# Optimization experiments

Measured on AMD Instinct MI355X. Metric: run time of the kernel, lower is better.

The kernel has to match this reference:

```python
import jax, jax.numpy as jnp
import numpy as np

N_NODES = 100_000
E_OFF = 1_000_000
HID = 32
GF = 8
NF = 8
N_LAYERS = 3


def _mlp(h, W1, b1, W2, b2):
    # Linear -> ReLU -> Linear (matches MLP([in, hidden, out]))
    return jax.nn.relu(h @ W1 + b1) @ W2 + b2


def _seg_mean(v, idx, n):
    s = jax.ops.segment_sum(v, idx, num_segments=n)
    c = jax.ops.segment_sum(jnp.ones((v.shape[0], 1), v.dtype), idx, num_segments=n)
    return s / jnp.maximum(c, 1.0)


def _graphnet(x, row, col, eattr2, g, p):
    # GraphNet with global block: edge MLP -> mean-aggregate to nodes -> node MLP -> global MLP
    eW1, eb1, eW2, eb2, nW1, nb1, nW2, nb2, gW1, gb1, gW2, gb2 = p
    n, e = x.shape[0], row.shape[0]
    gE = jnp.broadcast_to(g, (e, g.shape[1]))
    e_emb = _mlp(jnp.concatenate([gE, x[row], x[col], eattr2], axis=1), eW1, eb1, eW2, eb2)
    agg = _seg_mean(e_emb, row, n)
    gN = jnp.broadcast_to(g, (n, g.shape[1]))
    n_emb = _mlp(jnp.concatenate([gN, x, agg], axis=1), nW1, nb1, nW2, nb2)
    g_new = _mlp(jnp.concatenate([n_emb.mean(0, keepdims=True), e_emb.mean(0, keepdims=True), g], axis=1),
                 gW1, gb1, gW2, gb2)
    return e_emb, n_emb, g_new


def setup_inputs() -> dict:
    key = jax.random.key(0)
    ks = jax.random.split(key, 24)
    a = jax.random.randint(ks[0], (E_OFF,), 0, N_NODES)
    b = jax.random.randint(ks[1], (E_OFF,), 0, N_NODES)
    d = jnp.arange(N_NODES)
    l_ei = jnp.stack([jnp.concatenate([jnp.maximum(a, b), d]),
                      jnp.concatenate([jnp.minimum(a, b), d])])  # lower triangular + diag
    c = jax.random.randint(ks[2], (E_OFF,), 0, N_NODES)
    e = jax.random.randint(ks[3], (E_OFF,), 0, N_NODES)
    u_ei = jnp.stack([jnp.concatenate([jnp.minimum(c, e), d]),
                      jnp.concatenate([jnp.maximum(c, e), d])])  # upper triangular + diag
    E = E_OFF + N_NODES
    x = jax.random.normal(ks[4], (N_NODES, NF), dtype=jnp.float32)
    l_attr = jax.random.normal(ks[5], (E, 1), dtype=jnp.float32)
    u_attr = jax.random.normal(ks[6], (E, 1), dtype=jnp.float32)

    def w(k, shape):
        return (jax.random.normal(k, shape, dtype=jnp.float32) / np.sqrt(shape[-2])).astype(jnp.float32)

    e_in = GF + 2 * NF + 1 + 1  # 26 (edge attr padded to 2: skip col, zeros where absent)
    n_in = GF + 1 + NF          # 17
    g_in = NF + 1 + GF          # 17
    return {
        'x': x, 'l_edge_index': l_ei, 'u_edge_index': u_ei,
        'l_edge_attr': l_attr, 'u_edge_attr': u_attr,
        'eW1': w(ks[7], (2, N_LAYERS, e_in, HID)), 'eb1': 0.01 * jax.random.normal(ks[8], (2, N_LAYERS, HID)),
        'eW2': w(ks[9], (2, N_LAYERS, HID, 1)), 'eb2': 0.01 * jax.random.normal(ks[10], (2, N_LAYERS, 1)),
        'nW1': w(ks[11], (2, N_LAYERS, n_in, HID)), 'nb1': 0.01 * jax.random.normal(ks[12], (2, N_LAYERS, HID)),
        'nW2': w(ks[13], (2, N_LAYERS, HID, NF)), 'nb2': 0.01 * jax.random.normal(ks[14], (2, N_LAYERS, NF)),
        'gW1': w(ks[15], (2, N_LAYERS, g_in, HID)), 'gb1': 0.01 * jax.random.normal(ks[16], (2, N_LAYERS, HID)),
        'gW2': w(ks[17], (2, N_LAYERS, HID, GF)), 'gb2': 0.01 * jax.random.normal(ks[18], (2, N_LAYERS, GF)),
    }


def reference(x, l_edge_index, u_edge_index, l_edge_attr, u_edge_attr,
              eW1, eb1, eW2, eb2, nW1, nb1, nW2, nb2, gW1, gb1, gW2, gb2):
    params = (eW1, eb1, eW2, eb2, nW1, nb1, nW2, nb2, gW1, gb1, gW2, gb2)
    lr, lc = l_edge_index[0], l_edge_index[1]
    ur, uc = u_edge_index[0], u_edge_index[1]
    g = jnp.zeros((1, GF), x.dtype)
    l_e, u_e = l_edge_attr, u_edge_attr
    l_a = l_edge_attr  # skip-connection edge features (original matrix values)
    zl, zu = jnp.zeros_like(l_edge_attr), jnp.zeros_like(u_edge_attr)
    for i in range(N_LAYERS):
        p1 = tuple(w[0, i] for w in params)
        p2 = tuple(w[1, i] for w in params)
        l_in = jnp.concatenate([l_e, l_a if i != 0 else zl], axis=1)  # zeros col == no skip (block 0)
        l_e, l_n, g = _graphnet(x, lr, lc, l_in, g, p1)
        u_in = jnp.concatenate([u_e, zu], axis=1)  # l2 never has skip; padded zeros col
        u_e, u_n, g = _graphnet(l_n, ur, uc, u_in, g, p2)
        # NOTE: node embeddings are NOT carried across MP blocks in the original
    l_vals = jnp.where(lr == lc, jnp.exp(l_e[:, 0]), l_e[:, 0])
    u_vals = jnp.where(ur == uc, jnp.exp(u_e[:, 0]), u_e[:, 0])
    return jnp.concatenate([l_vals, u_vals])
```

## Files before the change

kernel.cpp:

```cpp
#include <hip/hip_runtime.h>


typedef unsigned int u32;

#define NB_SHIFT 9
#define NB_SIZE 512
#define RSTRIDE 1104

__device__ __forceinline__ float wave_sum(float v) {
#pragma unroll
    for (int off = 32; off > 0; off >>= 1) v += __shfl_down(v, off, 64);
    return v;
}


__global__ __launch_bounds__(256) void hist_kernel(
    const int* __restrict__ lr, const int* __restrict__ ur,
    u32* __restrict__ hist, int E, int B) {
    __shared__ u32 h[256];
    const int t = threadIdx.x;
    if (t < B) h[t] = 0;
    __syncthreads();
    const int s = blockIdx.y;
    const int* rows = s ? ur : lr;
    for (int i = blockIdx.x * 256 + t; i < E; i += gridDim.x * 256)
        atomicAdd(&h[rows[i] >> NB_SHIFT], 1u);
    __syncthreads();
    if (t < B && h[t]) atomicAdd(&hist[s * B + t], h[t]);
}

__global__ __launch_bounds__(256) void scan_kernel(
    const u32* __restrict__ hist, u32* __restrict__ offs,
    u32* __restrict__ cur, int B) {
    __shared__ u32 sh[256];
    const int t = threadIdx.x;
    for (int s = 0; s < 2; ++s) {
        const u32 v = (t < B) ? hist[s * B + t] : 0u;
        sh[t] = v;
        __syncthreads();
#pragma unroll
        for (int off = 1; off < 256; off <<= 1) {
            const u32 add = (t >= off) ? sh[t - off] : 0u;
            __syncthreads();
            sh[t] += add;
            __syncthreads();
        }
        const u32 exc = sh[t] - v;
        if (t < B) {
            offs[s * (B + 1) + t] = exc;
            cur[s * B + t] = exc;
        }
        if (t == 255) offs[s * (B + 1) + B] = sh[255];
        __syncthreads();
    }
}

#define SCHUNK 4096
__global__ __launch_bounds__(256) void scatter_kernel(
    const int* __restrict__ lr, const int* __restrict__ lc,
    const int* __restrict__ ur, const int* __restrict__ uc,
    const float* __restrict__ la, const float* __restrict__ ua,
    u32* __restrict__ cur, uint4* __restrict__ einfo, int E, int B) {
    __shared__ u32 lcnt[256], lbase[256];
    const int t = threadIdx.x;
    const int s = blockIdx.y;
    const int* rows = s ? ur : lr;
    const int* cols = s ? uc : lc;
    const float* attr = s ? ua : la;
    uint4* my = einfo + (size_t)s * E;
    if (t < B) lcnt[t] = 0;
    __syncthreads();
    const int base_e = blockIdx.x * SCHUNK;
#pragma unroll
    for (int k = 0; k < SCHUNK / 256; ++k) {
        const int e = base_e + k * 256 + t;
        if (e < E) atomicAdd(&lcnt[rows[e] >> NB_SHIFT], 1u);
    }
    __syncthreads();
    if (t < B) {
        const u32 c = lcnt[t];
        lbase[t] = c ? atomicAdd(&cur[s * B + t], c) : 0u;
        lcnt[t] = 0;
    }
    __syncthreads();
#pragma unroll
    for (int k = 0; k < SCHUNK / 256; ++k) {
        const int e = base_e + k * 256 + t;
        if (e < E) {
            const int r = rows[e];
            const int b = r >> NB_SHIFT;
            const u32 pos = lbase[b] + atomicAdd(&lcnt[b], 1u);
            my[pos] = make_uint4((u32)r, (u32)cols[e], (u32)e,
                                 __float_as_uint(attr[e]));
        }
    }
}


template <bool SKIP, bool FIRST, bool GAGG, bool VALS, bool STORE, bool GCOMP>
__global__ __launch_bounds__(512) void edge_kernel(
    const uint4* __restrict__ einfo,
    const float4* __restrict__ xf,
    const u32* __restrict__ offs,
    const float* __restrict__ eprev,
    const float* __restrict__ W1,
    const float* __restrict__ b1,
    const float* __restrict__ W2,
    const float* __restrict__ b2,
    const float* __restrict__ gprev,
    float* __restrict__ gout,
    const float* __restrict__ pebins,
    const float* __restrict__ pnbins,
    const float* __restrict__ gW1, const float* __restrict__ gb1,
    const float* __restrict__ gW2, const float* __restrict__ gb2,
    float* __restrict__ ebins,
    float* __restrict__ e_out,
    float* __restrict__ vals_out,
    int N, float inv_E) {
    __shared__ float asw[NB_SIZE * 32];
    const int t = threadIdx.x;
    const int b = blockIdx.x >> 1;

    if constexpr (GCOMP) {
        if (t < 64) {
            float nb[8];
#pragma unroll
            for (int q = 0; q < 8; ++q) nb[q] = pnbins[t * 16 + q];
            const float eb = pebins[t];
            float gin[17];
#pragma unroll
            for (int q = 0; q < 8; ++q) {
                const float s = wave_sum(nb[q]);
                gin[q] = __shfl(s, 0, 64) / (float)N;
            }
            const float es = wave_sum(eb);
            gin[8] = __shfl(es, 0, 64) * inv_E;
#pragma unroll
            for (int k = 0; k < 8; ++k) gin[9 + k] = gprev[k];
            float hv = 0.0f;
            if (t < 32) {
                hv = gb1[t];
#pragma unroll
                for (int k = 0; k < 17; ++k)
                    hv = fmaf(gin[k], gW1[k * 32 + t], hv);
                hv = fmaxf(hv, 0.0f);
            }
#pragma unroll
            for (int q = 0; q < 8; ++q) {
                const float c = (t < 32) ? hv * gW2[t * 8 + q] : 0.0f;
                const float s = wave_sum(c);
                if (t == 0) {
                    const float gv = gb2[q] + s;
                    asw[q] = gv;
                    if (blockIdx.x == 0) gout[q] = gv;
                }
            }
        }
    } else {
        if (t < 8) asw[t] = gprev[t];
    }
    __syncthreads();
    float gr[8];
#pragma unroll
    for (int k = 0; k < 8; ++k) gr[k] = asw[k];
    __syncthreads();

    const int n = (b << NB_SHIFT) + t;
    if (n < N) {
        const float4 x0 = xf[2 * (size_t)n], x1 = xf[2 * (size_t)n + 1];
        const float xs[8] = {x0.x, x0.y, x0.z, x0.w, x1.x, x1.y, x1.z, x1.w};
        float a[32];
#pragma unroll
        for (int j = 0; j < 32; ++j) {
            float v = b1[j];
#pragma unroll
            for (int k = 0; k < 8; ++k) v = fmaf(gr[k], W1[k * 32 + j], v);
            a[j] = v;
        }
        const float* __restrict__ WA = W1 + 8 * 32;
#pragma unroll
        for (int k = 0; k < 8; ++k) {
            const float v = xs[k];
#pragma unroll
            for (int j = 0; j < 32; ++j) a[j] = fmaf(v, WA[k * 32 + j], a[j]);
        }
        const int base = t * 32;
        const int sw = (t & 7) << 2;
#pragma unroll
        for (int q = 0; q < 8; ++q) {
            *(float4*)&asw[base + ((q * 4) ^ sw)] =
                make_float4(a[4 * q], a[4 * q + 1], a[4 * q + 2], a[4 * q + 3]);
        }
    }
    __syncthreads();

    const u32 beg = offs[b], end = offs[b + 1];
    const u32 len = end - beg;
    const u32 h0 = (len + 1) >> 1;
    const u32 hb = beg + ((blockIdx.x & 1) ? h0 : 0);
    const u32 he = (blockIdx.x & 1) ? end : beg + h0;
    const float* __restrict__ Wc = W1 + 16 * 32;
    const float* __restrict__ W24 = W1 + 24 * 32;
    const float* __restrict__ W25 = W1 + 25 * 32;
    float lsum = 0.0f;
    for (u32 i = hb + t; i < he; i += 512) {
        const uint4 e4 = einfo[i];
        const float attr = __uint_as_float(e4.w);
        float epv;
        if constexpr (FIRST) epv = attr;
        else epv = eprev[i];
        const u32 rl = e4.x & (NB_SIZE - 1);
        const int abase = rl * 32;
        const int asw_ = (rl & 7) << 2;
        float4 av[8];
#pragma unroll
        for (int q = 0; q < 8; ++q)
            av[q] = *(const float4*)&asw[abase + ((q * 4) ^ asw_)];
        const float4 xc0 = xf[2 * (size_t)e4.y];
        const float4 xc1 = xf[2 * (size_t)e4.y + 1];
        const float cx[8] = {xc0.x, xc0.y, xc0.z, xc0.w,
                             xc1.x, xc1.y, xc1.z, xc1.w};
        float hr[32];
#pragma unroll
        for (int q = 0; q < 8; ++q) {
            hr[4 * q + 0] = av[q].x; hr[4 * q + 1] = av[q].y;
            hr[4 * q + 2] = av[q].z; hr[4 * q + 3] = av[q].w;
        }
#pragma unroll
        for (int k = 0; k < 8; ++k) {
            const float v = cx[k];
#pragma unroll
            for (int j = 0; j < 32; ++j) hr[j] = fmaf(v, Wc[k * 32 + j], hr[j]);
        }
#pragma unroll
        for (int j = 0; j < 32; ++j) hr[j] = fmaf(epv, W24[j], hr[j]);
        if constexpr (SKIP) {
#pragma unroll
            for (int j = 0; j < 32; ++j) hr[j] = fmaf(attr, W25[j], hr[j]);
        }
        float out = b2[0];
#pragma unroll
        for (int j = 0; j < 32; ++j)
            out = fmaf(fmaxf(hr[j], 0.0f), W2[j], out);
        if constexpr (STORE) e_out[i] = out;
        if constexpr (VALS)
            vals_out[e4.z] = (e4.x == e4.y) ? expf(out) : out;
        if constexpr (GAGG) lsum += out;
    }
    if constexpr (GAGG) {
        __syncthreads();
        const float s = wave_sum(lsum);
        if ((t & 63) == 0) asw[t >> 6] = s;
        __syncthreads();
        if (t == 0) {
            float tot = 0.0f;
#pragma unroll
            for (int w = 0; w < 8; ++w) tot += asw[w];
            atomicAdd(&ebins[blockIdx.x & 63], tot);
        }
    }
}


template <bool COUNT, bool STORE_N>
__global__ __launch_bounds__(1024) void aggnode_kernel(
    const float* __restrict__ ep,
    const uint4* __restrict__ einfo,
    const u32* __restrict__ offs,
    const float4* __restrict__ xf,
    float* __restrict__ cntf,
    const float* __restrict__ g,
    const float* __restrict__ nW1, const float* __restrict__ nb1,
    const float* __restrict__ nW2, const float* __restrict__ nb2,
    float* __restrict__ n_out,
    float* __restrict__ nbins,
    int N) {
    __shared__ float sbin[NB_SIZE];
    __shared__ float cbin[NB_SIZE];
    __shared__ float biasN[32];
    __shared__ float npart[8][8];
    const int t = threadIdx.x;
    if (t < NB_SIZE) {
        sbin[t] = 0.0f;
        if constexpr (COUNT) cbin[t] = 0.0f;
    }
    if (t >= NB_SIZE && t < NB_SIZE + 32) {
        const int j = t - NB_SIZE;
        float v = nb1[j];
#pragma unroll
        for (int k = 0; k < 8; ++k) v = fmaf(g[k], nW1[k * 32 + j], v);
        biasN[j] = v;
    }
    __syncthreads();
    const int b = blockIdx.x;
    const u32 beg = offs[b], end = offs[b + 1];
    for (u32 i = beg + t; i < end; i += 1024) {
        const float v = ep[i];
        const u32 rl = einfo[i].x & (NB_SIZE - 1);
        atomicAdd(&sbin[rl], v);
        if constexpr (COUNT) atomicAdd(&cbin[rl], 1.0f);
    }
    __syncthreads();

    const int n0 = b << NB_SHIFT;
    float o[8];
    const bool active = (t < NB_SIZE) && (n0 + t < N);
    if (t < NB_SIZE) {
        const int n = n0 + t;
        const int idx = active ? n : (N - 1);
        float cntv;
        if constexpr (COUNT) {
            cntv = cbin[t];
            if (active) cntf[n] = cntv;
        } else {
            cntv = cntf[idx];
        }
        const float agg = sbin[t] / fmaxf(cntv, 1.0f);
        const float4 x0 = xf[2 * idx], x1 = xf[2 * idx + 1];
        float in[9] = {x0.x, x0.y, x0.z, x0.w, x1.x, x1.y, x1.z, x1.w, agg};
        float h[32];
#pragma unroll
        for (int j = 0; j < 8; ++j) {
            const float4 bb = reinterpret_cast<const float4*>(biasN)[j];
            h[4 * j + 0] = bb.x; h[4 * j + 1] = bb.y;
            h[4 * j + 2] = bb.z; h[4 * j + 3] = bb.w;
        }
        const float* __restrict__ Wk = nW1 + 8 * 32;
#pragma unroll
        for (int k = 0; k < 9; ++k) {
            const float v = in[k];
#pragma unroll
            for (int j = 0; j < 32; ++j) h[j] = fmaf(v, Wk[k * 32 + j], h[j]);
        }
#pragma unroll
        for (int q = 0; q < 8; ++q) o[q] = nb2[q];
#pragma unroll
        for (int j = 0; j < 32; ++j) {
            const float hv = fmaxf(h[j], 0.0f);
#pragma unroll
            for (int q = 0; q < 8; ++q) o[q] = fmaf(hv, nW2[j * 8 + q], o[q]);
        }
        if constexpr (STORE_N) {
            if (active) {
                reinterpret_cast<float4*>(n_out)[2 * n] =
                    make_float4(o[0], o[1], o[2], o[3]);
                reinterpret_cast<float4*>(n_out)[2 * n + 1] =
                    make_float4(o[4], o[5], o[6], o[7]);
            }
        }
#pragma unroll
        for (int q = 0; q < 8; ++q) {
            const float s = wave_sum(active ? o[q] : 0.0f);
            if ((t & 63) == 0) npart[t >> 6][q] = s;
        }
    }
    __syncthreads();
    if (t < 8) {
        float a = 0.0f;
#pragma unroll
        for (int w = 0; w < 8; ++w) a += npart[w][t];
        atomicAdd(&nbins[(b & 63) * 16 + t], a);
    }
}

extern "C" void kernel_launch(void* const* d_in, const int* in_sizes, int n_in,
                              void* d_out, int out_size, void* d_ws,
                              size_t ws_size, hipStream_t stream) {
    const float* x = (const float*)d_in[0];
    const int* l_ei = (const int*)d_in[1];
    const int* u_ei = (const int*)d_in[2];
    const float* l_attr = (const float*)d_in[3];
    const float* u_attr = (const float*)d_in[4];
    const float* eW1 = (const float*)d_in[5];
    const float* eb1 = (const float*)d_in[6];
    const float* eW2 = (const float*)d_in[7];
    const float* eb2 = (const float*)d_in[8];
    const float* nW1 = (const float*)d_in[9];
    const float* nb1 = (const float*)d_in[10];
    const float* nW2 = (const float*)d_in[11];
    const float* nb2 = (const float*)d_in[12];
    const float* gW1 = (const float*)d_in[13];
    const float* gb1 = (const float*)d_in[14];
    const float* gW2 = (const float*)d_in[15];
    const float* gb2 = (const float*)d_in[16];

    const int E = in_sizes[3];
    const int N = in_sizes[0] / 8;
    const int B = (N + NB_SIZE - 1) >> NB_SHIFT;
    const int Ep = (E + 3) & ~3;

    uint4* einfo = (uint4*)d_ws;
    float* l_e = (float*)(einfo + (size_t)2 * E);
    float* u_e = l_e + Ep;
    float* l_n = u_e + Ep;
    float* cnt_l = l_n + (size_t)8 * N;
    float* cnt_u = cnt_l + N;
    float* gslot = cnt_u + N;
    u32* hist = (u32*)(gslot + 56);
    float* dyn_all = (float*)(hist + 2 * B);
    u32* offs = (u32*)(dyn_all + 5 * RSTRIDE);
    u32* cur = offs + 2 * (B + 1);

    const int* lr = l_ei;
    const int* lc = l_ei + E;
    const int* ur = u_ei;
    const int* uc = u_ei + E;
    const int sg = (E + SCHUNK - 1) / SCHUNK;
    const float invE = 1.0f / (float)E;
    float* outL = (float*)d_out;
    float* outU = outL + E;
    const u32* offs_l = offs;
    const u32* offs_u = offs + (B + 1);

    hipMemsetAsync(gslot, 0, (size_t)(56 + 2 * B + 5 * RSTRIDE) * sizeof(float),
                   stream);
    hist_kernel<<<dim3(128, 2), 256, 0, stream>>>(lr, ur, hist, E, B);
    scan_kernel<<<1, 256, 0, stream>>>(hist, offs, cur, B);
    scatter_kernel<<<dim3(sg, 2), 256, 0, stream>>>(lr, lc, ur, uc, l_attr,
                                                    u_attr, cur, einfo, E, B);

    const size_t wsl[6] = {0, 3, 1, 4, 2, 5};

    for (int j = 0; j < 6; ++j) {
        const bool lower = !(j & 1);
        const size_t sl = wsl[j];
        float* ebins = dyn_all + (size_t)(j <= 4 ? j : 4) * RSTRIDE;
        float* nbins = ebins + 64;
        const float* pe = (j >= 1) ? dyn_all + (size_t)(j - 1) * RSTRIDE : nullptr;
        const float* pn = (j >= 1) ? pe + 64 : nullptr;
        const size_t psl = (j >= 1) ? wsl[j - 1] : 0;
        const float4* exf = (const float4*)(lower ? x : l_n);
        const uint4* einfo_t = einfo + (size_t)(lower ? 0 : 1) * E;
        const u32* eoffs = lower ? offs_l : offs_u;
        const float* eprev = lower ? l_e : u_e;
        float* e_out = lower ? l_e : u_e;
        const float* gprev = gslot + (size_t)(j >= 1 ? j - 1 : 0) * 8;
        float* gout = gslot + (size_t)j * 8;

#define EDGE_ARGS                                                             \
    einfo_t, exf, eoffs, eprev, eW1 + sl * 832, eb1 + sl * 32,                \
        eW2 + sl * 32, eb2 + sl, gprev, gout, pe, pn, gW1 + psl * 544,        \
        gb1 + psl * 32, gW2 + psl * 256, gb2 + psl * 8, ebins, e_out,         \
        (j == 4) ? outL : outU, N, invE

        switch (j) {
            case 0: edge_kernel<false, true, true, false, true, false>
                        <<<2 * B, 512, 0, stream>>>(EDGE_ARGS); break;
            case 1: edge_kernel<false, true, true, false, true, true>
                        <<<2 * B, 512, 0, stream>>>(EDGE_ARGS); break;
            case 2: edge_kernel<true, false, true, false, true, true>
                        <<<2 * B, 512, 0, stream>>>(EDGE_ARGS); break;
            case 3: edge_kernel<false, false, true, false, true, true>
                        <<<2 * B, 512, 0, stream>>>(EDGE_ARGS); break;
            case 4: edge_kernel<true, false, true, true, true, true>
                        <<<2 * B, 512, 0, stream>>>(EDGE_ARGS); break;
            case 5: edge_kernel<false, false, false, true, false, true>
                        <<<2 * B, 512, 0, stream>>>(EDGE_ARGS); break;
        }
#undef EDGE_ARGS

        if (j == 5) break;

        float* cntf = lower ? cnt_l : cnt_u;
        const float4* nxf = (const float4*)(lower ? x : l_n);

#define AGG_ARGS                                                              \
    e_out, einfo_t, eoffs, nxf, cntf, gslot + (size_t)j * 8, nW1 + sl * 544,  \
        nb1 + sl * 32, nW2 + sl * 256, nb2 + sl * 8, l_n, nbins, N

        switch (j) {
            case 0: aggnode_kernel<true, true>
                        <<<B, 1024, 0, stream>>>(AGG_ARGS); break;
            case 1: aggnode_kernel<true, false>
                        <<<B, 1024, 0, stream>>>(AGG_ARGS); break;
            case 2: aggnode_kernel<false, true>
                        <<<B, 1024, 0, stream>>>(AGG_ARGS); break;
            case 3: aggnode_kernel<false, false>
                        <<<B, 1024, 0, stream>>>(AGG_ARGS); break;
            case 4: aggnode_kernel<false, true>
                        <<<B, 1024, 0, stream>>>(AGG_ARGS); break;
        }
#undef AGG_ARGS
    }
}
```

Baseline: 606.4 us.

## Precompute per-node edge-MLP partials into a global table; flatten edge kernel grid

Splits the edge kernel. A new node kernel computes each node's row-side first-layer partial (global plus x[row] terms) once and writes it to a global table. The edge kernel then becomes a flat per-edge grid of 256-thread blocks that gathers that table instead of rebuilding it in LDS per bucket. Node buckets shrink from 512 to 256 with matching block sizes in the hist, scan, scatter and aggregation kernels. This trades LDS recomputation and uneven per-bucket load for an extra launch and a 32-float-per-node global gather per edge.

```diff
diff --git a/kernel.cpp b/kernel.cpp
--- a/kernel.cpp
+++ b/kernel.cpp
@@ -3,8 +3,8 @@
 
 typedef unsigned int u32;
 
-#define NB_SHIFT 9
-#define NB_SIZE 512
+#define NB_SHIFT 8
+#define NB_SIZE 256
 #define RSTRIDE 1104
 
 __device__ __forceinline__ float wave_sum(float v) {
@@ -14,32 +14,32 @@
 }
 
 
-__global__ __launch_bounds__(256) void hist_kernel(
+__global__ __launch_bounds__(512) void hist_kernel(
     const int* __restrict__ lr, const int* __restrict__ ur,
     u32* __restrict__ hist, int E, int B) {
-    __shared__ u32 h[256];
+    __shared__ u32 h[512];
     const int t = threadIdx.x;
     if (t < B) h[t] = 0;
     __syncthreads();
     const int s = blockIdx.y;
     const int* rows = s ? ur : lr;
-    for (int i = blockIdx.x * 256 + t; i < E; i += gridDim.x * 256)
+    for (int i = blockIdx.x * 512 + t; i < E; i += gridDim.x * 512)
         atomicAdd(&h[rows[i] >> NB_SHIFT], 1u);
     __syncthreads();
     if (t < B && h[t]) atomicAdd(&hist[s * B + t], h[t]);
 }
 
-__global__ __launch_bounds__(256) void scan_kernel(
+__global__ __launch_bounds__(512) void scan_kernel(
     const u32* __restrict__ hist, u32* __restrict__ offs,
     u32* __restrict__ cur, int B) {
-    __shared__ u32 sh[256];
+    __shared__ u32 sh[512];
     const int t = threadIdx.x;
     for (int s = 0; s < 2; ++s) {
         const u32 v = (t < B) ? hist[s * B + t] : 0u;
         sh[t] = v;
         __syncthreads();
 #pragma unroll
-        for (int off = 1; off < 256; off <<= 1) {
+        for (int off = 1; off < 512; off <<= 1) {
             const u32 add = (t >= off) ? sh[t - off] : 0u;
             __syncthreads();
             sh[t] += add;
@@ -50,18 +50,18 @@
             offs[s * (B + 1) + t] = exc;
             cur[s * B + t] = exc;
         }
-        if (t == 255) offs[s * (B + 1) + B] = sh[255];
+        if (t == 511) offs[s * (B + 1) + B] = sh[511];
         __syncthreads();
     }
 }
 
 #define SCHUNK 4096
-__global__ __launch_bounds__(256) void scatter_kernel(
+__global__ __launch_bounds__(512) void scatter_kernel(
     const int* __restrict__ lr, const int* __restrict__ lc,
     const int* __restrict__ ur, const int* __restrict__ uc,
     const float* __restrict__ la, const float* __restrict__ ua,
     u32* __restrict__ cur, uint4* __restrict__ einfo, int E, int B) {
-    __shared__ u32 lcnt[256], lbase[256];
+    __shared__ u32 lcnt[512], lbase[512];
     const int t = threadIdx.x;
     const int s = blockIdx.y;
     const int* rows = s ? ur : lr;
@@ -72,8 +72,8 @@
     __syncthreads();
     const int base_e = blockIdx.x * SCHUNK;
 #pragma unroll
-    for (int k = 0; k < SCHUNK / 256; ++k) {
-        const int e = base_e + k * 256 + t;
+    for (int k = 0; k < SCHUNK / 512; ++k) {
+        const int e = base_e + k * 512 + t;
         if (e < E) atomicAdd(&lcnt[rows[e] >> NB_SHIFT], 1u);
     }
     __syncthreads();
@@ -84,8 +84,8 @@
     }
     __syncthreads();
 #pragma unroll
-    for (int k = 0; k < SCHUNK / 256; ++k) {
-        const int e = base_e + k * 256 + t;
+    for (int k = 0; k < SCHUNK / 512; ++k) {
+        const int e = base_e + k * 512 + t;
         if (e < E) {
             const int r = rows[e];
             const int b = r >> NB_SHIFT;
@@ -97,30 +97,19 @@
 }
 
 
-template <bool SKIP, bool FIRST, bool GAGG, bool VALS, bool STORE, bool GCOMP>
-__global__ __launch_bounds__(512) void edge_kernel(
-    const uint4* __restrict__ einfo,
-    const float4* __restrict__ xf,
-    const u32* __restrict__ offs,
-    const float* __restrict__ eprev,
-    const float* __restrict__ W1,
+template <bool GCOMP>
+__global__ __launch_bounds__(256) void nodew_kernel(
+    const float4* __restrict__ xf, const float* __restrict__ W1,
     const float* __restrict__ b1,
-    const float* __restrict__ W2,
-    const float* __restrict__ b2,
     const float* __restrict__ gprev,
     float* __restrict__ gout,
     const float* __restrict__ pebins,
     const float* __restrict__ pnbins,
     const float* __restrict__ gW1, const float* __restrict__ gb1,
     const float* __restrict__ gW2, const float* __restrict__ gb2,
-    float* __restrict__ ebins,
-    float* __restrict__ e_out,
-    float* __restrict__ vals_out,
-    int N, float inv_E) {
-    __shared__ float asw[NB_SIZE * 32];
-    const int t = threadIdx.x;
-    const int b = blockIdx.x >> 1;
-
+    float4* __restrict__ Atab, int N, float inv_E) {
+    __shared__ float gsh[8];
+    const int t = threadIdx.x;
     if constexpr (GCOMP) {
         if (t < 64) {
             float nb[8];
@@ -151,119 +140,119 @@
                 const float s = wave_sum(c);
                 if (t == 0) {
                     const float gv = gb2[q] + s;
-                    asw[q] = gv;
+                    gsh[q] = gv;
                     if (blockIdx.x == 0) gout[q] = gv;
                 }
             }
         }
     } else {
-        if (t < 8) asw[t] = gprev[t];
-    }
-    __syncthreads();
+        if (t < 8) gsh[t] = gprev[t];
+    }
+    __syncthreads();
+    const int n = blockIdx.x * 256 + t;
+    if (n >= N) return;
     float gr[8];
 #pragma unroll
-    for (int k = 0; k < 8; ++k) gr[k] = asw[k];
-    __syncthreads();
-
-    const int n = (b << NB_SHIFT) + t;
-    if (n < N) {
-        const float4 x0 = xf[2 * (size_t)n], x1 = xf[2 * (size_t)n + 1];
-        const float xs[8] = {x0.x, x0.y, x0.z, x0.w, x1.x, x1.y, x1.z, x1.w};
-        float a[32];
-#pragma unroll
-        for (int j = 0; j < 32; ++j) {
-            float v = b1[j];
-#pragma unroll
-            for (int k = 0; k < 8; ++k) v = fmaf(gr[k], W1[k * 32 + j], v);
-            a[j] = v;
-        }
-        const float* __restrict__ WA = W1 + 8 * 32;
-#pragma unroll
-        for (int k = 0; k < 8; ++k) {
-            const float v = xs[k];
-#pragma unroll
-            for (int j = 0; j < 32; ++j) a[j] = fmaf(v, WA[k * 32 + j], a[j]);
-        }
-        const int base = t * 32;
-        const int sw = (t & 7) << 2;
-#pragma unroll
-        for (int q = 0; q < 8; ++q) {
-            *(float4*)&asw[base + ((q * 4) ^ sw)] =
-                make_float4(a[4 * q], a[4 * q + 1], a[4 * q + 2], a[4 * q + 3]);
-        }
-    }
-    __syncthreads();
-
-    const u32 beg = offs[b], end = offs[b + 1];
-    const u32 len = end - beg;
-    const u32 h0 = (len + 1) >> 1;
-    const u32 hb = beg + ((blockIdx.x & 1) ? h0 : 0);
-    const u32 he = (blockIdx.x & 1) ? end : beg + h0;
+    for (int k = 0; k < 8; ++k) gr[k] = gsh[k];
+    const float4 x0 = xf[2 * (size_t)n], x1 = xf[2 * (size_t)n + 1];
+    const float xs[8] = {x0.x, x0.y, x0.z, x0.w, x1.x, x1.y, x1.z, x1.w};
+    float a[32];
+#pragma unroll
+    for (int j = 0; j < 32; ++j) {
+        float v = b1[j];
+#pragma unroll
+        for (int k = 0; k < 8; ++k) v = fmaf(gr[k], W1[k * 32 + j], v);
+        a[j] = v;
+    }
+    const float* __restrict__ WA = W1 + 8 * 32;
+#pragma unroll
+    for (int k = 0; k < 8; ++k) {
+        const float v = xs[k];
+#pragma unroll
+        for (int j = 0; j < 32; ++j) a[j] = fmaf(v, WA[k * 32 + j], a[j]);
+    }
+    float4* An = Atab + 8 * (size_t)n;
+#pragma unroll
+    for (int q = 0; q < 8; ++q)
+        An[q] = make_float4(a[4 * q], a[4 * q + 1], a[4 * q + 2], a[4 * q + 3]);
+}
+
+
+template <bool SKIP, bool FIRST, bool GAGG, bool VALS, bool STORE>
+__global__ __launch_bounds__(256) void edge_kernel(
+    const uint4* __restrict__ einfo,
+    const float4* __restrict__ Atab,
+    const float4* __restrict__ xf,
+    const float* __restrict__ eprev,
+    const float* __restrict__ W1,
+    const float* __restrict__ W2,
+    const float* __restrict__ b2,
+    float* __restrict__ ebins,
+    float* __restrict__ e_out,
+    float* __restrict__ vals_out,
+    int E, int cpx) {
+    __shared__ float wpart[4];
+    const int t = threadIdx.x;
+    const int lid = (blockIdx.x & 7) * cpx + (blockIdx.x >> 3);
+    const int i0 = lid * 256;
+    if (i0 >= E) return;
+    const int i = i0 + t;
+    const bool valid = i < E;
+    const int idx = valid ? i : i0;
+
+    const uint4 e4 = einfo[idx];
+    const float attr = __uint_as_float(e4.w);
+    float epv;
+    if constexpr (FIRST) epv = attr;
+    else epv = eprev[idx];
+    const float4* __restrict__ Ar = Atab + 8 * (size_t)e4.x;
+    float h[32];
+#pragma unroll
+    for (int q = 0; q < 8; ++q) {
+        const float4 av = Ar[q];
+        h[4 * q + 0] = av.x; h[4 * q + 1] = av.y;
+        h[4 * q + 2] = av.z; h[4 * q + 3] = av.w;
+    }
+    const float4 xc0 = xf[2 * (size_t)e4.y], xc1 = xf[2 * (size_t)e4.y + 1];
+    const float cx[8] = {xc0.x, xc0.y, xc0.z, xc0.w,
+                         xc1.x, xc1.y, xc1.z, xc1.w};
     const float* __restrict__ Wc = W1 + 16 * 32;
+#pragma unroll
+    for (int k = 0; k < 8; ++k) {
+        const float v = cx[k];
+#pragma unroll
+        for (int j = 0; j < 32; ++j) h[j] = fmaf(v, Wc[k * 32 + j], h[j]);
+    }
     const float* __restrict__ W24 = W1 + 24 * 32;
-    const float* __restrict__ W25 = W1 + 25 * 32;
-    float lsum = 0.0f;
-    for (u32 i = hb + t; i < he; i += 512) {
-        const uint4 e4 = einfo[i];
-        const float attr = __uint_as_float(e4.w);
-        float epv;
-        if constexpr (FIRST) epv = attr;
-        else epv = eprev[i];
-        const u32 rl = e4.x & (NB_SIZE - 1);
-        const int abase = rl * 32;
-        const int asw_ = (rl & 7) << 2;
-        float4 av[8];
-#pragma unroll
-        for (int q = 0; q < 8; ++q)
-            av[q] = *(const float4*)&asw[abase + ((q * 4) ^ asw_)];
-        const float4 xc0 = xf[2 * (size_t)e4.y];
-        const float4 xc1 = xf[2 * (size_t)e4.y + 1];
-        const float cx[8] = {xc0.x, xc0.y, xc0.z, xc0.w,
-                             xc1.x, xc1.y, xc1.z, xc1.w};
-        float hr[32];
-#pragma unroll
-        for (int q = 0; q < 8; ++q) {
-            hr[4 * q + 0] = av[q].x; hr[4 * q + 1] = av[q].y;
-            hr[4 * q + 2] = av[q].z; hr[4 * q + 3] = av[q].w;
-        }
-#pragma unroll
-        for (int k = 0; k < 8; ++k) {
-            const float v = cx[k];
-#pragma unroll
-            for (int j = 0; j < 32; ++j) hr[j] = fmaf(v, Wc[k * 32 + j], hr[j]);
-        }
-#pragma unroll
-        for (int j = 0; j < 32; ++j) hr[j] = fmaf(epv, W24[j], hr[j]);
-        if constexpr (SKIP) {
-#pragma unroll
-            for (int j = 0; j < 32; ++j) hr[j] = fmaf(attr, W25[j], hr[j]);
-        }
-        float out = b2[0];
-#pragma unroll
-        for (int j = 0; j < 32; ++j)
-            out = fmaf(fmaxf(hr[j], 0.0f), W2[j], out);
+#pragma unroll
+    for (int j = 0; j < 32; ++j) h[j] = fmaf(epv, W24[j], h[j]);
+    if constexpr (SKIP) {
+        const float* __restrict__ W25 = W1 + 25 * 32;
+#pragma unroll
+        for (int j = 0; j < 32; ++j) h[j] = fmaf(attr, W25[j], h[j]);
+    }
+    float out = b2[0];
+#pragma unroll
+    for (int j = 0; j < 32; ++j) out = fmaf(fmaxf(h[j], 0.0f), W2[j], out);
+
+    if (valid) {
         if constexpr (STORE) e_out[i] = out;
         if constexpr (VALS)
             vals_out[e4.z] = (e4.x == e4.y) ? expf(out) : out;
-        if constexpr (GAGG) lsum += out;
     }
     if constexpr (GAGG) {
+        const float s = wave_sum(valid ? out : 0.0f);
+        if ((t & 63) == 0) wpart[t >> 6] = s;
         __syncthreads();
-        const float s = wave_sum(lsum);
-        if ((t & 63) == 0) asw[t >> 6] = s;
-        __syncthreads();
-        if (t == 0) {
-            float tot = 0.0f;
-#pragma unroll
-            for (int w = 0; w < 8; ++w) tot += asw[w];
-            atomicAdd(&ebins[blockIdx.x & 63], tot);
-        }
+        if (t == 0)
+            atomicAdd(&ebins[lid & 63],
+                      wpart[0] + wpart[1] + wpart[2] + wpart[3]);
     }
 }
 
 
 template <bool COUNT, bool STORE_N>
-__global__ __launch_bounds__(1024) void aggnode_kernel(
+__global__ __launch_bounds__(512) void aggnode_kernel(
     const float* __restrict__ ep,
     const uint4* __restrict__ einfo,
     const u32* __restrict__ offs,
@@ -278,7 +267,7 @@
     __shared__ float sbin[NB_SIZE];
     __shared__ float cbin[NB_SIZE];
     __shared__ float biasN[32];
-    __shared__ float npart[8][8];
+    __shared__ float npart[4][8];
     const int t = threadIdx.x;
     if (t < NB_SIZE) {
         sbin[t] = 0.0f;
@@ -294,7 +283,7 @@
     __syncthreads();
     const int b = blockIdx.x;
     const u32 beg = offs[b], end = offs[b + 1];
-    for (u32 i = beg + t; i < end; i += 1024) {
+    for (u32 i = beg + t; i < end; i += 512) {
         const float v = ep[i];
         const u32 rl = einfo[i].x & (NB_SIZE - 1);
         atomicAdd(&sbin[rl], v);
@@ -358,7 +347,7 @@
     if (t < 8) {
         float a = 0.0f;
 #pragma unroll
-        for (int w = 0; w < 8; ++w) a += npart[w][t];
+        for (int w = 0; w < 4; ++w) a += npart[w][t];
         atomicAdd(&nbins[(b & 63) * 16 + t], a);
     }
 }
@@ -390,7 +379,8 @@
     const int Ep = (E + 3) & ~3;
 
     uint4* einfo = (uint4*)d_ws;
-    float* l_e = (float*)(einfo + (size_t)2 * E);
+    float* Atab = (float*)(einfo + (size_t)2 * E);
+    float* l_e = Atab + (size_t)32 * N;
     float* u_e = l_e + Ep;
     float* l_n = u_e + Ep;
     float* cnt_l = l_n + (size_t)8 * N;
@@ -406,6 +396,10 @@
     const int* ur = u_ei;
     const int* uc = u_ei + E;
     const int sg = (E + SCHUNK - 1) / SCHUNK;
+    const int ng = (N + 255) / 256;
+    const int eg = (E + 255) / 256;
+    const int nwg8 = (eg + 7) & ~7;
+    const int cpx = nwg8 >> 3;
     const float invE = 1.0f / (float)E;
     float* outL = (float*)d_out;
     float* outU = outL + E;
@@ -414,9 +408,9 @@
 
     hipMemsetAsync(gslot, 0, (size_t)(56 + 2 * B + 5 * RSTRIDE) * sizeof(float),
                    stream);
-    hist_kernel<<<dim3(128, 2), 256, 0, stream>>>(lr, ur, hist, E, B);
-    scan_kernel<<<1, 256, 0, stream>>>(hist, offs, cur, B);
-    scatter_kernel<<<dim3(sg, 2), 256, 0, stream>>>(lr, lc, ur, uc, l_attr,
+    hist_kernel<<<dim3(64, 2), 512, 0, stream>>>(lr, ur, hist, E, B);
+    scan_kernel<<<1, 512, 0, stream>>>(hist, offs, cur, B);
+    scatter_kernel<<<dim3(sg, 2), 512, 0, stream>>>(lr, lc, ur, uc, l_attr,
                                                     u_attr, cur, einfo, E, B);
 
     const size_t wsl[6] = {0, 3, 1, 4, 2, 5};
@@ -437,25 +431,33 @@
         const float* gprev = gslot + (size_t)(j >= 1 ? j - 1 : 0) * 8;
         float* gout = gslot + (size_t)j * 8;
 
+        if (j == 0)
+            nodew_kernel<false><<<ng, 256, 0, stream>>>(
+                exf, eW1 + sl * 832, eb1 + sl * 32, gprev, gout, pe, pn,
+                gW1, gb1, gW2, gb2, (float4*)Atab, N, invE);
+        else
+            nodew_kernel<true><<<ng, 256, 0, stream>>>(
+                exf, eW1 + sl * 832, eb1 + sl * 32, gprev, gout, pe, pn,
+                gW1 + psl * 544, gb1 + psl * 32, gW2 + psl * 256,
+                gb2 + psl * 8, (float4*)Atab, N, invE);
+
 #define EDGE_ARGS                                                             \
-    einfo_t, exf, eoffs, eprev, eW1 + sl * 832, eb1 + sl * 32,                \
-        eW2 + sl * 32, eb2 + sl, gprev, gout, pe, pn, gW1 + psl * 544,        \
-        gb1 + psl * 32, gW2 + psl * 256, gb2 + psl * 8, ebins, e_out,         \
-        (j == 4) ? outL : outU, N, invE
+    einfo_t, (const float4*)Atab, exf, eprev, eW1 + sl * 832,                 \
+        eW2 + sl * 32, eb2 + sl, ebins, e_out, (j == 4) ? outL : outU, E, cpx
 
         switch (j) {
-            case 0: edge_kernel<false, true, true, false, true, false>
-                        <<<2 * B, 512, 0, stream>>>(EDGE_ARGS); break;
-            case 1: edge_kernel<false, true, true, false, true, true>
-                        <<<2 * B, 512, 0, stream>>>(EDGE_ARGS); break;
-            case 2: edge_kernel<true, false, true, false, true, true>
-                        <<<2 * B, 512, 0, stream>>>(EDGE_ARGS); break;
-            case 3: edge_kernel<false, false, true, false, true, true>
-                        <<<2 * B, 512, 0, stream>>>(EDGE_ARGS); break;
-            case 4: edge_kernel<true, false, true, true, true, true>
-                        <<<2 * B, 512, 0, stream>>>(EDGE_ARGS); break;
-            case 5: edge_kernel<false, false, false, true, false, true>
-                        <<<2 * B, 512, 0, stream>>>(EDGE_ARGS); break;
+            case 0: edge_kernel<false, true, true, false, true>
+                        <<<nwg8, 256, 0, stream>>>(EDGE_ARGS); break;
+            case 1: edge_kernel<false, true, true, false, true>
+                        <<<nwg8, 256, 0, stream>>>(EDGE_ARGS); break;
+            case 2: edge_kernel<true, false, true, false, true>
+                        <<<nwg8, 256, 0, stream>>>(EDGE_ARGS); break;
+            case 3: edge_kernel<false, false, true, false, true>
+                        <<<nwg8, 256, 0, stream>>>(EDGE_ARGS); break;
+            case 4: edge_kernel<true, false, true, true, true>
+                        <<<nwg8, 256, 0, stream>>>(EDGE_ARGS); break;
+            case 5: edge_kernel<false, false, false, true, false>
+                        <<<nwg8, 256, 0, stream>>>(EDGE_ARGS); break;
         }
 #undef EDGE_ARGS
 
@@ -470,15 +472,15 @@
 
         switch (j) {
             case 0: aggnode_kernel<true, true>
-                        <<<B, 1024, 0, stream>>>(AGG_ARGS); break;
+                        <<<B, 512, 0, stream>>>(AGG_ARGS); break;
             case 1: aggnode_kernel<true, false>
-                        <<<B, 1024, 0, stream>>>(AGG_ARGS); break;
+                        <<<B, 512, 0, stream>>>(AGG_ARGS); break;
             case 2: aggnode_kernel<false, true>
-                        <<<B, 1024, 0, stream>>>(AGG_ARGS); break;
+                        <<<B, 512, 0, stream>>>(AGG_ARGS); break;
             case 3: aggnode_kernel<false, false>
-                        <<<B, 1024, 0, stream>>>(AGG_ARGS); break;
+                        <<<B, 512, 0, stream>>>(AGG_ARGS); break;
             case 4: aggnode_kernel<false, true>
-                        <<<B, 1024, 0, stream>>>(AGG_ARGS); break;
+                        <<<B, 512, 0, stream>>>(AGG_ARGS); break;
         }
 #undef AGG_ARGS
     }
```

New measurement: 549.5 us. -9.4%, faster.
